# Kernel tuning notes

Measured on AMD Instinct MI355X. Metric: run time of the kernel, lower is better.

Reference implementation:

```python
import jax, jax.numpy as jnp
import numpy as np

EPS = 1e-6
HID = 2048; N_HEADS = 16; Q_LORA = 768; KV_LORA = 512
ROPE_D = 64; NOPE_D = 128; V_D = 128
IDX_H = 32; IDX_D = 128; IDX_TOPK = 512
N_EXP = 8; TOPK = 4; N_GROUP = 4; TOPK_GROUP = 2
MOE_I = 512; SHARED_I = 512; ROUTED_SCALE = 2.5
T = 1024
NEG = -1e30


def _rms(x, w, eps=EPS):
    x = x.astype(jnp.float32)
    return x * jax.lax.rsqrt(jnp.mean(x * x, axis=-1, keepdims=True) + eps) * w


def _ln(x, w, b, eps=EPS):
    x = x.astype(jnp.float32)
    m = jnp.mean(x, axis=-1, keepdims=True)
    v = jnp.mean((x - m) ** 2, axis=-1, keepdims=True)
    return (x - m) * jax.lax.rsqrt(v + eps) * w + b


def _rope_cs(positions, dim):
    inv = 1.0 / (10000.0 ** (jnp.arange(0, dim, 2, dtype=jnp.float32) / dim))
    f = positions.astype(jnp.float32)[:, None] * inv[None, :]  # [T, dim/2]
    return jnp.cos(f), jnp.sin(f)


def _rope(x, cos, sin):
    # neox-style rotate-half over last dim
    d = x.shape[-1] // 2
    x1, x2 = x[..., :d], x[..., d:]
    while cos.ndim < x.ndim:
        cos, sin = cos[:, None], sin[:, None]
    return jnp.concatenate([x1 * cos - x2 * sin, x2 * cos + x1 * sin], axis=-1)


def setup_inputs() -> dict:
    key = jax.random.key(0)
    ks = iter(jax.random.split(key, 32))
    w = lambda *s: jax.random.normal(next(ks), s, jnp.float32) * 0.02
    inp = {
        'positions': jnp.arange(T, dtype=jnp.int32),
        'hidden_states': jax.random.normal(next(ks), (T, HID), jnp.float32),
        'residual': jax.random.normal(next(ks), (T, HID), jnp.float32),
        'w_input_ln': jnp.ones((HID,), jnp.float32),
        'w_post_ln': jnp.ones((HID,), jnp.float32),
        'w_step1': w(Q_LORA + KV_LORA + ROPE_D + IDX_D + IDX_H, HID),
        'w_q_a_ln': jnp.ones((Q_LORA,), jnp.float32),
        'w_kv_a_ln': jnp.ones((KV_LORA,), jnp.float32),
        'idx_k_ln_w': jnp.ones((IDX_D,), jnp.float32),
        'idx_k_ln_b': jnp.zeros((IDX_D,), jnp.float32),
        'w_step3': w(IDX_H * IDX_D + N_HEADS * (NOPE_D + ROPE_D), Q_LORA),
        'W_UK_T': w(N_HEADS, NOPE_D, KV_LORA),
        'W_UV': w(N_HEADS, KV_LORA, V_D),
        'w_o': w(HID, N_HEADS * V_D),
        'gate_w': w(N_EXP, HID),
        'gate_bias': jnp.zeros((N_EXP,), jnp.float32),
        'shared_gate_up': w(2 * SHARED_I, HID),
        'shared_down': w(HID, SHARED_I),
        'exp_gate_up': w(N_EXP, 2 * MOE_I, HID),
        'exp_down': w(N_EXP, HID, MOE_I),
    }
    return inp


def reference(positions, hidden_states, residual, w_input_ln, w_post_ln, w_step1,
              w_q_a_ln, w_kv_a_ln, idx_k_ln_w, idx_k_ln_b, w_step3, W_UK_T, W_UV,
              w_o, gate_w, gate_bias, shared_gate_up, shared_down, exp_gate_up, exp_down):
    Tn = hidden_states.shape[0]
    rows = jnp.arange(Tn)
    # (allreduce is identity at tp=1) + residual add + RMSNorm
    res = hidden_states.astype(jnp.float32) + residual.astype(jnp.float32)
    h = _rms(res, w_input_ln)
    # ---- Step 1: fused qkv_a + indexer_wk + indexer_weights_proj GEMM ----
    s1 = h @ w_step1.T
    o0 = 0
    q_c = s1[:, o0:o0 + Q_LORA]; o0 += Q_LORA
    kv_c = s1[:, o0:o0 + KV_LORA]; o0 += KV_LORA
    k_pe = s1[:, o0:o0 + ROPE_D]; o0 += ROPE_D
    idx_k = s1[:, o0:o0 + IDX_D]; o0 += IDX_D
    idx_w_raw = s1[:, o0:o0 + IDX_H]
    cos, sin = _rope_cs(positions, ROPE_D)
    # fused_norm_rope: norms + rope on k_pe / indexer-k
    q_c = _rms(q_c, w_q_a_ln)
    kv_c = _rms(kv_c, w_kv_a_ln)
    k_pe = _rope(k_pe, cos, sin)
    idx_k = _ln(idx_k, idx_k_ln_w, idx_k_ln_b)
    idx_k = jnp.concatenate([_rope(idx_k[:, :ROPE_D], cos, sin), idx_k[:, ROPE_D:]], axis=-1)
    # ---- Step 3: fused indexer_wq_b + q_b_proj GEMM ----
    s3 = q_c @ w_step3.T
    idx_q = s3[:, :IDX_H * IDX_D].reshape(Tn, IDX_H, IDX_D)
    q = s3[:, IDX_H * IDX_D:].reshape(Tn, N_HEADS, NOPE_D + ROPE_D)
    q_nope, q_pe = q[..., :NOPE_D], q[..., NOPE_D:]
    # absorb W_UK: [T,H,nope] x [H,nope,kv_lora] -> [T,H,kv_lora]
    ql_nope = jnp.einsum('thn,hnk->thk', q_nope, W_UK_T)
    q_pe = _rope(q_pe, cos, sin)
    idx_q = jnp.concatenate([_rope(idx_q[..., :ROPE_D], cos, sin), idx_q[..., ROPE_D:]], axis=-1)
    idx_q = idx_q * (IDX_D ** -0.5)            # indexer softmax scale
    idx_w = idx_w_raw * (IDX_H ** -0.5)        # per-head weights scale
    # ---- sparse attention indexer: relu(q.k) head-weighted sum, causal top-k ----
    il = jnp.einsum('thd,sd->ths', idx_q, idx_k)          # [T,Hi,S]
    iscores = jnp.einsum('ths,th->ts', jax.nn.relu(il), idx_w)
    causal = positions[:, None] >= positions[None, :]
    iscores = jnp.where(causal, iscores, NEG)
    topk_idx = jax.lax.top_k(iscores, IDX_TOPK)[1]        # [T, IDX_TOPK]
    tmask = jnp.zeros((Tn, Tn), bool).at[rows[:, None], topk_idx].set(True)
    mask = causal & tmask
    # ---- MLA MQA attention in latent space ----
    mqa_q = jnp.concatenate([ql_nope, jnp.broadcast_to(q_pe, (Tn, N_HEADS, ROPE_D))], axis=-1)
    kv = jnp.concatenate([kv_c, k_pe], axis=-1)           # [S, kv_lora+rope]
    att = jnp.einsum('thd,sd->hts', mqa_q, kv) * ((NOPE_D + ROPE_D) ** -0.5)
    att = jnp.where(mask[None], att, NEG)
    p = jax.nn.softmax(att, axis=-1)
    o = jnp.einsum('hts,sk->thk', p, kv_c)                # [T,H,kv_lora]
    o = jnp.einsum('thk,hkv->thv', o, W_UV).reshape(Tn, N_HEADS * V_D)
    attn_out = o @ w_o.T
    # add + RMSNorm
    res2 = attn_out + res
    h2 = _rms(res2, w_post_ln)
    # ---- MoE: DeepSeekV3 sigmoid grouped routing + shared experts ----
    glog = h2 @ gate_w.T
    sg = jax.nn.sigmoid(glog)
    sc = sg + gate_bias
    gsz = N_EXP // N_GROUP
    grp = sc.reshape(Tn, N_GROUP, gsz)
    grp_score = jax.lax.top_k(grp, min(2, gsz))[0].sum(-1)
    gidx = jax.lax.top_k(grp_score, TOPK_GROUP)[1]
    gmask = jnp.zeros((Tn, N_GROUP), bool).at[rows[:, None], gidx].set(True)
    emask = jnp.repeat(gmask, gsz, axis=1)
    sc_m = jnp.where(emask, sc, NEG)
    _, tid = jax.lax.top_k(sc_m, TOPK)
    tw = jnp.take_along_axis(sg, tid, axis=1)
    tw = tw / (tw.sum(-1, keepdims=True) + 1e-20) * ROUTED_SCALE
    comb = jnp.zeros((Tn, N_EXP), jnp.float32).at[rows[:, None], tid].set(tw)
    # routed experts (dense masked combine as reference for grouped-GEMM dispatch)
    gu = jnp.einsum('th,eih->tei', h2, exp_gate_up)       # [T,E,2I]
    act = jax.nn.silu(gu[..., :MOE_I]) * gu[..., MOE_I:]
    routed_e = jnp.einsum('tei,ehi->teh', act, exp_down)  # [T,E,H]
    routed = jnp.einsum('te,teh->th', comb, routed_e)
    # shared experts
    gus = h2 @ shared_gate_up.T
    shared = (jax.nn.silu(gus[:, :SHARED_I]) * gus[:, SHARED_I:]) @ shared_down.T
    out = shared + routed
    return out, res2
```

## Files before the change

### kernel.cpp

```cpp
#include <hip/hip_runtime.h>
#include <math.h>

static constexpr int TT  = 1024;
static constexpr int HID = 2048;
static constexpr int NH  = 16;
static constexpr int QL  = 768;
static constexpr int KVL = 512;
static constexpr int RD  = 64;
static constexpr int IH  = 32;
static constexpr int ID  = 128;
static constexpr int S1W = QL + KVL + RD + ID + IH;
static constexpr int S3W = IH*ID + NH*(128+RD);

#define SCALE_ATT 0.07216878364870323f
#define SC_IDXQ   0.08838834764831845f
#define SC_IDXW   0.17677669529663687f
#define NEGR      -1e30f
#define NEGL      -3.0e38f

typedef __bf16 bf16x8 __attribute__((ext_vector_type(8)));
typedef float  f32x4  __attribute__((ext_vector_type(4)));

#define GLD_LDS16(g, l) __builtin_amdgcn_global_load_lds( \
    (const __attribute__((address_space(1))) void*)(g),   \
    (__attribute__((address_space(3))) void*)(l), 16, 0, 0)

__device__ __forceinline__ unsigned short f2b(float x) {
  union { float f; unsigned u; } v; v.f = x;
  unsigned r = v.u + 0x7FFFu + ((v.u >> 16) & 1u);
  return (unsigned short)(r >> 16);
}
__device__ __forceinline__ float b2f(unsigned short u) {
  union { unsigned u; float f; } v; v.u = ((unsigned)u) << 16;
  return v.f;
}

__device__ __forceinline__ float blk_sum256(float v, float* s) {
  #pragma unroll
  for (int o = 32; o > 0; o >>= 1) v += __shfl_down(v, o, 64);
  __syncthreads();
  if ((threadIdx.x & 63) == 0) s[threadIdx.x >> 6] = v;
  __syncthreads();
  return s[0] + s[1] + s[2] + s[3];
}

__global__ __launch_bounds__(256) void k_prelude(const float* __restrict__ hs,
                                                 const float* __restrict__ rsd,
                                                 const float* __restrict__ w,
                                                 float* __restrict__ res,
                                                 unsigned short* __restrict__ hb) {
  int t = blockIdx.x;
  __shared__ float scr[4];
  float vals[8]; float ss = 0.f;
  #pragma unroll
  for (int r = 0; r < 8; r++) {
    int d = threadIdx.x + 256*r;
    float v = hs[(size_t)t*HID + d] + rsd[(size_t)t*HID + d];
    vals[r] = v; res[(size_t)t*HID + d] = v; ss = fmaf(v, v, ss);
  }
  ss = blk_sum256(ss, scr);
  float inv = 1.f/sqrtf(ss/(float)HID + 1e-6f);
  #pragma unroll
  for (int r = 0; r < 8; r++) {
    int d = threadIdx.x + 256*r;
    hb[(size_t)t*HID + d] = f2b(vals[r]*inv*w[d]);
  }
}

__global__ __launch_bounds__(256) void k_res2(const float* __restrict__ attn1,
                                              const float* __restrict__ attn2,
                                              const float* __restrict__ res,
                                              const float* __restrict__ w,
                                              float* __restrict__ res2_out,
                                              float* __restrict__ h2,
                                              unsigned short* __restrict__ h2b) {
  int t = blockIdx.x;
  __shared__ float scr[4];
  float vals[8]; float ss = 0.f;
  #pragma unroll
  for (int r = 0; r < 8; r++) {
    int d = threadIdx.x + 256*r;
    float v = attn1[(size_t)t*HID + d] + attn2[(size_t)t*HID + d] + res[(size_t)t*HID + d];
    vals[r] = v; res2_out[(size_t)t*HID + d] = v; ss = fmaf(v, v, ss);
  }
  ss = blk_sum256(ss, scr);
  float inv = 1.f/sqrtf(ss/(float)HID + 1e-6f);
  #pragma unroll
  for (int r = 0; r < 8; r++) {
    int d = threadIdx.x + 256*r;
    float o = vals[r]*inv*w[d];
    h2[(size_t)t*HID + d] = o;
    h2b[(size_t)t*HID + d] = f2b(o);
  }
}

__global__ void k_ropecs(const int* __restrict__ pos, float* __restrict__ cosb, float* __restrict__ sinb) {
  int i = blockIdx.x*256 + threadIdx.x;
  if (i >= TT*32) return;
  int t = i >> 5, k = i & 31;
  double inv = pow(10000.0, -((double)(2*k))/64.0);
  double f = (double)pos[t] * inv;
  cosb[i] = (float)cos(f);
  sinb[i] = (float)sin(f);
}

__global__ void k_f2b(const float* __restrict__ s, unsigned short* __restrict__ d,
                      long long n, long long ntot) {
  long long stride = (long long)gridDim.x * 1024;
  for (long long i = ((long long)blockIdx.x*256 + threadIdx.x)*4; i < ntot; i += stride) {
    float x0, x1, x2, x3;
    if (i + 3 < n) { float4 v = *(const float4*)(s + i); x0=v.x; x1=v.y; x2=v.z; x3=v.w; }
    else {
      x0 = (i   < n) ? s[i]   : 0.f; x1 = (i+1 < n) ? s[i+1] : 0.f;
      x2 = (i+2 < n) ? s[i+2] : 0.f; x3 = (i+3 < n) ? s[i+3] : 0.f;
    }
    ushort4 o; o.x=f2b(x0); o.y=f2b(x1); o.z=f2b(x2); o.w=f2b(x3);
    *(ushort4*)(d + i) = o;
  }
}

__global__ void k_f2b4(const float* __restrict__ s0, unsigned short* __restrict__ d0, long long n0,
                       const float* __restrict__ s1, unsigned short* __restrict__ d1, long long n1,
                       const float* __restrict__ s2, unsigned short* __restrict__ d2, long long n2,
                       const float* __restrict__ s3, unsigned short* __restrict__ d3, long long n3) {
  long long ntot = n0 + n1 + n2 + n3;
  long long stride = (long long)gridDim.x * 1024;
  for (long long i = ((long long)blockIdx.x*256 + threadIdx.x)*4; i < ntot; i += stride) {
    const float* s; unsigned short* d; long long j = i;
    if (j < n0) { s = s0; d = d0; }
    else { j -= n0;
      if (j < n1) { s = s1; d = d1; }
      else { j -= n1;
        if (j < n2) { s = s2; d = d2; }
        else { j -= n2; s = s3; d = d3; } } }
    float4 v = *(const float4*)(s + j);
    ushort4 o; o.x=f2b(v.x); o.y=f2b(v.y); o.z=f2b(v.z); o.w=f2b(v.w);
    *(ushort4*)(d + j) = o;
  }
}

__global__ __launch_bounds__(256) void k_tconvb(const float* __restrict__ src,
                                                unsigned short* __restrict__ dst,
                                                int R, int C) {
  src += (size_t)blockIdx.z * R * C;
  dst += (size_t)blockIdx.z * R * C;
  __shared__ float tile[32][33];
  int c0 = blockIdx.x * 32, r0 = blockIdx.y * 32;
  int tx = threadIdx.x & 31, ty = threadIdx.x >> 5;
  #pragma unroll
  for (int i = 0; i < 4; i++) {
    int r = r0 + ty + i*8;
    tile[ty + i*8][tx] = src[(size_t)r*C + c0 + tx];
  }
  __syncthreads();
  #pragma unroll
  for (int i = 0; i < 4; i++) {
    int c = c0 + ty + i*8;
    dst[(size_t)c*R + r0 + tx] = f2b(tile[tx][ty + i*8]);
  }
}

template<int BM, int OUT, bool ILV, int MOE>
__global__ __launch_bounds__(256) void k_mgemm(
    const unsigned short* __restrict__ A, int lda, long long sA,
    const unsigned short* __restrict__ B, int ldb, long long sB,
    void* __restrict__ Cv, int ldc, long long sC,
    int N, int K, float alpha, int cskip, int ktri,
    int nseg, long long segA, long long segB,
    const float* __restrict__ comb,
    const int* __restrict__ cntp, const int* __restrict__ tokp) {
  constexpr int MR  = BM / 32;
  constexpr int ITA = BM / 32;
  const int row0 = blockIdx.y * BM;
  const int col0 = blockIdx.x * 128;
  if (cskip >= 0 && col0 > row0 + cskip) return;
  const int zb = blockIdx.z;
  int cnt = 0; long long off = 0;
  if (MOE) {
    cnt = cntp[zb];
    for (int e = 0; e < zb; e++) off += cntp[e];
    if (row0 >= cnt) return;
  }
  __shared__ __align__(16) unsigned short As[2][BM*64];
  __shared__ __align__(16) unsigned short Bs[2][128*64];
  const int tid  = threadIdx.x;
  const int wave = tid >> 6, lane = tid & 63;
  const int wm = wave >> 1, wn = wave & 1;
  A += (size_t)zb * (size_t)sA;
  B += (size_t)zb * (size_t)sB;
  if (MOE == 2) A += off * (long long)lda;

  int tki[ITA];
  if (MOE == 1) {
    #pragma unroll
    for (int it = 0; it < ITA; it++) {
      int r = (wave*64 + it*256 + lane) >> 3;
      tki[it] = tokp[zb*1024 + row0 + r];
    }
  }

  f32x4 acc[MR][4] = {};
  const int l15 = lane & 15, l4 = lane >> 4;
  const int sx = l15 & 7;
  int Kend = K;
  if (ktri) {
    int kub = (((row0 + BM - 1) >> 7) + 1) << 7;
    if (kub < Kend) Kend = kub;
  }
  const int nk = Kend >> 6;
  const int nt = nseg * nk;

  auto STAGE = [&](int b, const unsigned short* Ab, const unsigned short* Bb, int k0) {
    #pragma unroll
    for (int it = 0; it < ITA; it++) {
      int base = wave*64 + it*256;
      int sidx = base + lane;
      int r = sidx >> 3, s = sidx & 7;
      int s_src = s ^ (r & 7);
      const unsigned short* ga;
      if (MOE == 1) ga = Ab + (size_t)tki[it]*lda + k0 + s_src*8;
      else          ga = Ab + (size_t)(row0 + r)*lda + k0 + s_src*8;
      GLD_LDS16(ga, &As[b][base*8]);
    }
    #pragma unroll
    for (int it = 0; it < 4; it++) {
      int base = wave*64 + it*256;
      int sidx = base + lane;
      int r = sidx >> 3, s = sidx & 7;
      int s_src = s ^ (r & 7);
      int rt = col0 + r;
      int srow = ILV ? ((rt >> 1) + (rt & 1)*512) : rt;
      const unsigned short* gb = Bb + (size_t)srow*ldb + k0 + s_src*8;
      GLD_LDS16(gb, &Bs[b][base*8]);
    }
  };

  STAGE(0, A, B, 0);
  int ks = 64, sg = 0;
  if (ks == Kend) { ks = 0; sg = 1; }
  __syncthreads();
  int cur = 0;

  for (int u = 0; u < nt; u++) {
    if (u + 1 < nt) {
      STAGE(cur ^ 1, A + (size_t)sg*segA, B + (size_t)sg*segB, ks);
      ks += 64;
      if (ks == Kend) { ks = 0; sg++; }
    }
    #pragma unroll
    for (int kc = 0; kc < 2; kc++) {
      const int sl = ((kc*4 + l4) ^ sx) << 3;
      bf16x8 fa[MR], fb[4];
      #pragma unroll
      for (int mf = 0; mf < MR; mf++)
        fa[mf] = *(const bf16x8*)&As[cur][(wm*(BM/2) + mf*16 + l15)*64 + sl];
      #pragma unroll
      for (int nf = 0; nf < 4; nf++)
        fb[nf] = *(const bf16x8*)&Bs[cur][(wn*64 + nf*16 + l15)*64 + sl];
      #pragma unroll
      for (int mf = 0; mf < MR; mf++)
        #pragma unroll
        for (int nf = 0; nf < 4; nf++)
          acc[mf][nf] = __builtin_amdgcn_mfma_f32_16x16x32_bf16(fa[mf], fb[nf], acc[mf][nf], 0, 0, 0);
    }
    __syncthreads();
    cur ^= 1;
  }

  #pragma unroll
  for (int mf = 0; mf < MR; mf++) {
    #pragma unroll
    for (int nf = 0; nf < 4; nf++) {
      int n = col0 + wn*64 + nf*16 + l15;
      #pragma unroll
      for (int r = 0; r < 4; r++) {
        int m = row0 + wm*(BM/2) + mf*16 + l4*4 + r;
        float v = acc[mf][nf][r] * alpha;
        if (OUT == 2) {
          float p = __shfl_xor(v, 1, 64);
          if ((l15 & 1) == 0) {
            bool ok = true;
            long long mrow = m;
            float w;
            if (MOE == 1) {
              ok = (m < cnt); mrow = off + m;
              int tok = tokp[zb*1024 + m];
              w = (zb < 8) ? comb[tok*8 + zb] : 1.f;
            } else {
              w = (zb < 8) ? comb[m*8 + zb] : 1.f;
            }
            if (ok) {
              float rres = v/(1.f + expf(-v)) * p * w;
              ((unsigned short*)Cv)[(size_t)zb*sC + (size_t)mrow*ldc + (n >> 1)] = f2b(rres);
            }
          }
        } else if (n < N) {
          bool ok = true;
          long long mrow = m;
          if (MOE == 2) { ok = (m < cnt); mrow = off + m; }
          if (ok) {
            size_t idx = (size_t)mrow*ldc + n;
            if (OUT == 1) ((unsigned short*)Cv)[(size_t)zb*sC + idx] = f2b(v);
            else          ((float*)Cv)[(size_t)zb*sC + idx] = v;
          }
        }
      }
    }
  }
}

__global__ __launch_bounds__(256) void k_post1(const float* __restrict__ s1a,
    const float* __restrict__ s1b,
    const float* __restrict__ wq, const float* __restrict__ wkv,
    const float* __restrict__ lnw, const float* __restrict__ lnb,
    const float* __restrict__ cosb, const float* __restrict__ sinb,
    unsigned short* __restrict__ qcb, float* __restrict__ kvc, float* __restrict__ kpe,
    float* __restrict__ idxk, float* __restrict__ idxw) {
  int t = blockIdx.x, tid = threadIdx.x;
  __shared__ float rowb[S1W];
  __shared__ float scr[4];
  __shared__ float yb[128];
  for (int d = tid; d < S1W; d += 256)
    rowb[d] = s1a[(size_t)t*S1W + d] + s1b[(size_t)t*S1W + d];
  __syncthreads();
  float ss = 0.f;
  for (int d = tid; d < QL; d += 256) { float v = rowb[d]; ss = fmaf(v,v,ss); }
  ss = blk_sum256(ss, scr);
  float inv = 1.f/sqrtf(ss/(float)QL + 1e-6f);
  for (int d = tid; d < QL; d += 256) qcb[(size_t)t*QL + d] = f2b(rowb[d]*inv*wq[d]);
  ss = 0.f;
  for (int d = tid; d < KVL; d += 256) { float v = rowb[QL+d]; ss = fmaf(v,v,ss); }
  ss = blk_sum256(ss, scr);
  inv = 1.f/sqrtf(ss/(float)KVL + 1e-6f);
  for (int d = tid; d < KVL; d += 256) kvc[(size_t)t*KVL + d] = rowb[QL+d]*inv*wkv[d];
  float sm = (tid < 128) ? rowb[1344 + tid] : 0.f;
  float tot = blk_sum256(sm, scr);
  float mean = tot / 128.f;
  float vs = 0.f;
  if (tid < 128) { float v = rowb[1344+tid] - mean; vs = v*v; }
  vs = blk_sum256(vs, scr);
  float ivn = 1.f/sqrtf(vs/128.f + 1e-6f);
  if (tid < 128) yb[tid] = (rowb[1344+tid]-mean)*ivn*lnw[tid] + lnb[tid];
  __syncthreads();
  if (tid < 32) {
    float c = cosb[t*32 + tid], s = sinb[t*32 + tid];
    idxk[(size_t)t*ID + tid]      = yb[tid]*c - yb[32+tid]*s;
    idxk[(size_t)t*ID + 32 + tid] = yb[32+tid]*c + yb[tid]*s;
    float x1 = rowb[1280+tid], x2 = rowb[1312+tid];
    kpe[(size_t)t*RD + tid]      = x1*c - x2*s;
    kpe[(size_t)t*RD + 32 + tid] = x2*c + x1*s;
    idxw[(size_t)t*IH + tid] = rowb[1472+tid] * SC_IDXW;
  } else if (tid >= 64 && tid < 128) {
    idxk[(size_t)t*ID + tid] = yb[tid];
  }
}

__global__ __launch_bounds__(256) void k_post3b(const float* __restrict__ s3,
                                                const float* __restrict__ cosb,
                                                const float* __restrict__ sinb,
                                                unsigned short* __restrict__ s3b) {
  int t = blockIdx.x, tid = threadIdx.x;
  const float* row = s3 + (size_t)t*S3W;
  __shared__ float buf[S3W];
  __shared__ float cs[32], sn[32];
  if (tid < 32) { cs[tid] = cosb[t*32+tid]; sn[tid] = sinb[t*32+tid]; }
  for (int d = tid; d < S3W; d += 256) buf[d] = row[d];
  __syncthreads();
  for (int p = tid; p < 1024; p += 256) {
    int h = p >> 5, d = p & 31;
    float c = cs[d], s = sn[d];
    float x1 = buf[h*ID + d], x2 = buf[h*ID + 32 + d];
    buf[h*ID + d]      = (x1*c - x2*s) * SC_IDXQ;
    buf[h*ID + 32 + d] = (x2*c + x1*s) * SC_IDXQ;
  }
  for (int p = tid; p < 2048; p += 256) {
    int h = p >> 6, d = 64 + (p & 63);
    buf[h*ID + d] *= SC_IDXQ;
  }
  for (int p = tid; p < 512; p += 256) {
    int h = p >> 5, d = p & 31;
    float c = cs[d], s = sn[d];
    int base = IH*ID + h*192 + 128;
    float x1 = buf[base + d], x2 = buf[base + 32 + d];
    buf[base + d]      = x1*c - x2*s;
    buf[base + 32 + d] = x2*c + x1*s;
  }
  __syncthreads();
  unsigned short* orow = s3b + (size_t)t*S3W;
  for (int g = tid*4; g < S3W; g += 1024) {
    ushort4 o;
    o.x = f2b(buf[g]); o.y = f2b(buf[g+1]); o.z = f2b(buf[g+2]); o.w = f2b(buf[g+3]);
    *(ushort4*)(orow + g) = o;
  }
}

__global__ void k_qpe(const unsigned short* __restrict__ s3b, unsigned short* __restrict__ qm) {
  int i = blockIdx.x*256 + threadIdx.x;
  int t = i >> 10, r = i & 1023;
  int h = r >> 6, j = r & 63;
  float v = b2f(s3b[(size_t)t*S3W + IH*ID + h*192 + 128 + j]) * SCALE_ATT;
  qm[(size_t)t*9216 + h*576 + 512 + j] = f2b(v);
}

__global__ void k_kvb(const float* __restrict__ kvc, const float* __restrict__ kpe,
                      unsigned short* __restrict__ kvb) {
  int i = blockIdx.x*256 + threadIdx.x;
  int s = i / 576, d = i - s*576;
  float v = (d < 512) ? kvc[(size_t)s*KVL + d] : kpe[(size_t)s*RD + (d - 512)];
  kvb[i] = f2b(v);
}

__global__ __launch_bounds__(256) void k_ired(const float* __restrict__ il,
                                              const float* __restrict__ idxw,
                                              float* __restrict__ isc,
                                              int first, int last, int h0) {
  int tr = blockIdx.x;
  int t = 512 + tr;
  int s0 = threadIdx.x * 4;
  float4 acc;
  if (first) acc = make_float4(0.f, 0.f, 0.f, 0.f);
  else       acc = *(float4*)(isc + (size_t)tr*TT + s0);
  #pragma unroll
  for (int hh = 0; hh < 8; hh++) {
    float w = idxw[t*IH + h0 + hh];
    float4 v = *(const float4*)(il + (size_t)hh*524288 + (size_t)tr*1024 + s0);
    acc.x += fmaxf(v.x, 0.f) * w;
    acc.y += fmaxf(v.y, 0.f) * w;
    acc.z += fmaxf(v.z, 0.f) * w;
    acc.w += fmaxf(v.w, 0.f) * w;
  }
  if (last) {
    if (s0     > t) acc.x = NEGR;
    if (s0 + 1 > t) acc.y = NEGR;
    if (s0 + 2 > t) acc.z = NEGR;
    if (s0 + 3 > t) acc.w = NEGR;
  }
  *(float4*)(isc + (size_t)tr*TT + s0) = acc;
}

__global__ __launch_bounds__(512) void k_topk(const float* __restrict__ isc,
                                              unsigned char* __restrict__ mask) {
  int t = 512 + blockIdx.x;
  const float* row = isc + (size_t)blockIdx.x * TT;
  __shared__ unsigned long long keys[1024];
  int tid = threadIdx.x;
  for (int i = tid; i < 1024; i += 512) {
    float v = row[i];
    unsigned int b = __float_as_uint(v);
    unsigned int u = (b & 0x80000000u) ? ~b : (b | 0x80000000u);
    keys[i] = ((unsigned long long)u << 32) | (unsigned int)(1023 - i);
  }
  __syncthreads();
  for (int k = 2; k <= 1024; k <<= 1) {
    for (int j = k >> 1; j > 0; j >>= 1) {
      int i = ((tid & ~(j - 1)) << 1) | (tid & (j - 1));
      int l = i | j;
      unsigned long long a = keys[i], b = keys[l];
      bool up = ((i & k) == 0);
      if ((a < b) == up) { keys[i] = b; keys[l] = a; }
      __syncthreads();
    }
  }
  unsigned char* mrow = mask + (size_t)t * TT;
  for (int p = tid; p < 1024; p += 512) {
    int s = 1023 - (int)(keys[p] & 0xFFFFFFFFu);
    mrow[s] = (p < 512) ? (unsigned char)1 : (unsigned char)0;
  }
}

__global__ __launch_bounds__(256) void k_psoft(unsigned short* __restrict__ pb,
                                               const unsigned char* __restrict__ mask) {
  int b = blockIdx.x;
  int t = b & 1023, h = b >> 10;
  unsigned short* row = pb + ((size_t)h << 20) + ((size_t)t << 10);
  int tid = threadIdx.x;
  __shared__ float scr[4];
  int s0 = tid * 4;
  int rub = ((t >> 7) + 1) << 7;
  bool act = (s0 < rub);
  float v0 = 0.f, v1 = 0.f, v2 = 0.f, v3 = 0.f;
  bool m0 = false, m1 = false, m2 = false, m3 = false;
  if (act) {
    ushort4 raw = *(const ushort4*)(row + s0);
    v0 = b2f(raw.x); v1 = b2f(raw.y); v2 = b2f(raw.z); v3 = b2f(raw.w);
    if (t < 512) {
      m0 = (s0 <= t); m1 = (s0+1 <= t); m2 = (s0+2 <= t); m3 = (s0+3 <= t);
    } else {
      uchar4 mk = *(const uchar4*)(mask + (size_t)t*TT + s0);
      m0 = (s0 <= t) && mk.x; m1 = (s0+1 <= t) && mk.y;
      m2 = (s0+2 <= t) && mk.z; m3 = (s0+3 <= t) && mk.w;
    }
  }
  float mx = NEGL;
  if (m0) mx = v0;
  if (m1) mx = fmaxf(mx, v1);
  if (m2) mx = fmaxf(mx, v2);
  if (m3) mx = fmaxf(mx, v3);
  #pragma unroll
  for (int o = 32; o > 0; o >>= 1) mx = fmaxf(mx, __shfl_down(mx, o, 64));
  __syncthreads();
  if ((tid & 63) == 0) scr[tid >> 6] = mx;
  __syncthreads();
  mx = fmaxf(fmaxf(scr[0], scr[1]), fmaxf(scr[2], scr[3]));
  float p0 = m0 ? expf(v0 - mx) : 0.f;
  float p1 = m1 ? expf(v1 - mx) : 0.f;
  float p2 = m2 ? expf(v2 - mx) : 0.f;
  float p3 = m3 ? expf(v3 - mx) : 0.f;
  float sum = blk_sum256((p0+p1)+(p2+p3), scr);
  float inv = 1.f / sum;
  if (act) {
    ushort4 o;
    o.x = f2b(p0*inv); o.y = f2b(p1*inv); o.z = f2b(p2*inv); o.w = f2b(p3*inv);
    *(ushort4*)(row + s0) = o;
  }
}

__global__ __launch_bounds__(256) void k_gate(const float* __restrict__ h2,
                                              const float* __restrict__ gw,
                                              const float* __restrict__ gb,
                                              float* __restrict__ comb) {
  int t = blockIdx.x, tid = threadIdx.x;
  int e = tid >> 5, lane = tid & 31;
  __shared__ float gl[8];
  float p = 0.f;
  for (int d = lane; d < HID; d += 32) p = fmaf(h2[(size_t)t*HID+d], gw[(size_t)e*HID+d], p);
  #pragma unroll
  for (int o = 16; o > 0; o >>= 1) p += __shfl_down(p, o, 32);
  if (lane == 0) gl[e] = p;
  __syncthreads();
  if (tid == 0) {
    float sg[8], sc[8];
    #pragma unroll
    for (int i = 0; i < 8; i++) { sg[i] = 1.f/(1.f+expf(-gl[i])); sc[i] = sg[i] + gb[i]; }
    float gs[4];
    #pragma unroll
    for (int g = 0; g < 4; g++) gs[g] = sc[2*g] + sc[2*g+1];
    int g0 = 0;
    for (int g = 1; g < 4; g++) if (gs[g] > gs[g0]) g0 = g;
    int g1 = -1;
    for (int g = 0; g < 4; g++) { if (g == g0) continue; if (g1 < 0 || gs[g] > gs[g1]) g1 = g; }
    float wsum = 1e-20f;
    #pragma unroll
    for (int i = 0; i < 8; i++) { int g = i >> 1; if (g == g0 || g == g1) wsum += sg[i]; }
    #pragma unroll
    for (int i = 0; i < 8; i++) { int g = i >> 1; comb[t*8+i] = (g == g0 || g == g1) ? sg[i]/wsum*2.5f : 0.f; }
  }
}

__global__ __launch_bounds__(1024) void k_route(const float* __restrict__ comb,
                                                int* __restrict__ tokidx,
                                                int* __restrict__ rank,
                                                int* __restrict__ cntp) {
  int e = blockIdx.x;
  int t = threadIdx.x;
  if (e == 8) {
    tokidx[8*1024 + t] = t;
    if (t == 0) cntp[8] = 1024;
    return;
  }
  int lane = t & 63, w = t >> 6;
  bool sel = comb[t*8 + e] != 0.0f;
  unsigned long long bal = __ballot(sel);
  int pw = __popcll(bal & ((1ull << lane) - 1ull));
  int wt = __popcll(bal);
  __shared__ int wsum[16];
  if (lane == 0) wsum[w] = wt;
  __syncthreads();
  int woff = 0, total = 0;
  #pragma unroll
  for (int i = 0; i < 16; i++) { int v = wsum[i]; if (i < w) woff += v; total += v; }
  int pos = woff + pw;
  rank[t*8 + e] = sel ? pos : -1;
  if (sel) tokidx[e*1024 + pos] = t;
  __syncthreads();
  if (t >= total) tokidx[e*1024 + t] = 0;
  if (t == 0) cntp[e] = total;
}

__global__ __launch_bounds__(256) void k_rsum(const float* __restrict__ dpc,
                                              const int* __restrict__ rank,
                                              const int* __restrict__ cntp,
                                              float* __restrict__ out) {
  int t = blockIdx.x;
  int d = threadIdx.x * 8;
  int offs[8]; int acc_off = 0;
  #pragma unroll
  for (int e = 0; e < 8; e++) { offs[e] = acc_off; acc_off += cntp[e]; }
  const float* ps = dpc + (size_t)(acc_off + t)*2048 + d;
  float4 a0 = *(const float4*)ps;
  float4 a1 = *(const float4*)(ps + 4);
  #pragma unroll
  for (int e = 0; e < 8; e++) {
    int r = rank[t*8 + e];
    if (r >= 0) {
      const float* p = dpc + (size_t)(offs[e] + r)*2048 + d;
      float4 b0 = *(const float4*)p;
      float4 b1 = *(const float4*)(p + 4);
      a0.x += b0.x; a0.y += b0.y; a0.z += b0.z; a0.w += b0.w;
      a1.x += b1.x; a1.y += b1.y; a1.z += b1.z; a1.w += b1.w;
    }
  }
  float* po = out + (size_t)t*2048 + d;
  *(float4*)po = a0;
  *(float4*)(po + 4) = a1;
}

extern "C" void kernel_launch(void* const* d_in, const int* in_sizes, int n_in,
                              void* d_out, int out_size, void* d_ws, size_t ws_size,
                              hipStream_t stream) {
  const int*   positions = (const int*)d_in[0];
  const float* hs     = (const float*)d_in[1];
  const float* rsd    = (const float*)d_in[2];
  const float* w_in   = (const float*)d_in[3];
  const float* w_post = (const float*)d_in[4];
  const float* w_s1   = (const float*)d_in[5];
  const float* w_qln  = (const float*)d_in[6];
  const float* w_kvln = (const float*)d_in[7];
  const float* iklnw  = (const float*)d_in[8];
  const float* iklnb  = (const float*)d_in[9];
  const float* w_s3   = (const float*)d_in[10];
  const float* wukt   = (const float*)d_in[11];
  const float* wuv    = (const float*)d_in[12];
  const float* w_o    = (const float*)d_in[13];
  const float* gate_w = (const float*)d_in[14];
  const float* gate_b = (const float*)d_in[15];
  const float* sh_gu  = (const float*)d_in[16];
  const float* sh_dn  = (const float*)d_in[17];
  const float* ex_gu  = (const float*)d_in[18];
  const float* ex_dn  = (const float*)d_in[19];

  float* ws = (float*)d_ws;
  typedef unsigned short ush;
  float* RES   = ws + 0;
  float* COSB  = ws + 2097152;
  float* SINB  = ws + 2129920;
  float* KVC   = ws + 2162688;
  float* KPE   = ws + 2686976;
  float* IDXK  = ws + 2752512;
  float* IDXW  = ws + 2883584;
  float* COMB  = ws + 2916352;
  ush*   HB    = (ush*)(ws + 2924544);
  ush*   WS1B  = (ush*)(ws + 3973120);
  float* S1P0  = ws + 5545984;
  ush*   QCB   = (ush*)(ws + 7086080);
  ush*   WS3B  = (ush*)(ws + 7479296);
  ush*   WOB   = (ush*)(ws + 7479296);
  float* S3    = ws + 10231808;
  float* S1P1  = ws + 10231808;
  ush*   S3B   = (ush*)(ws + 17571840);
  ush*   WUKTB = (ush*)(ws + 21241856);
  ush*   QMQAB = (ush*)(ws + 21766144);
  float* ISC   = ws + 26484736;
  unsigned char* MASK = (unsigned char*)(ws + 27009024);
  ush*   WUVB  = (ush*)(ws + 27271168);
  ush*   KVB   = (ush*)(ws + 27795456);
  ush*   VTB   = (ush*)(ws + 28090368);
  ush*   O2B   = (ush*)(ws + 28352512);
  float* ILB   = ws + 27795456;
  ush*   IDXKB = (ush*)(ws + 31989760);
  ush*   PB    = (ush*)(ws + 10231808);
  ush*   OHB   = (ush*)(ws + 18620416);
  float* ATTNP = ws + 10231808;
  float* H2     = ws + 2924544;
  ush*   H2B    = (ush*)(ws + 5021696);
  ush*   EXGUB  = (ush*)(ws + 6070272);
  ush*   SHGUB  = (ush*)(ws + 14458880);
  ush*   EXDNB  = (ush*)(ws + 15507456);
  ush*   SHDNB  = (ush*)(ws + 19701760);
  ush*   ACTC   = (ush*)(ws + 20226048);
  float* DPC    = ws + 21536768;
  int*   TOKIDX = (int*)(ws + 32022528);
  int*   RANK   = (int*)(ws + 32031744);
  int*   CNT    = (int*)(ws + 32039936);

  float* OUT0 = (float*)d_out;
  float* OUT_RES2 = OUT0 + (size_t)TT*HID;

  k_prelude<<<TT, 256, 0, stream>>>(hs, rsd, w_in, RES, HB);
  k_ropecs<<<(TT*32)/256, 256, 0, stream>>>(positions, COSB, SINB);
  k_f2b<<<1024, 256, 0, stream>>>(w_s1, WS1B, 3080192LL, 3145728LL);
  k_f2b<<<1024, 256, 0, stream>>>(w_s3, WS3B, 5505024LL, 5505024LL);
  k_tconvb<<<dim3(16,4,16), 256, 0, stream>>>(wukt, WUKTB, 128, 512);
  k_tconvb<<<dim3(4,16,16), 256, 0, stream>>>(wuv, WUVB, 512, 128);
  k_mgemm<64,0,false,0><<<dim3(12,16,2), 256, 0, stream>>>(
      HB, 2048, 1024, WS1B, 2048, 1024, S1P0, S1W, 4685824,
      1504, 1024, 1.f, -1, 0, 1, 0, 0, nullptr, nullptr, nullptr);
  k_post1<<<TT, 256, 0, stream>>>(S1P0, S1P1, w_qln, w_kvln, iklnw, iklnb, COSB, SINB, QCB, KVC, KPE, IDXK, IDXW);
  k_f2b<<<128, 256, 0, stream>>>(IDXK, IDXKB, 131072LL, 131072LL);
  k_mgemm<64,0,false,0><<<dim3(56,16,1), 256, 0, stream>>>(
      QCB, 768, 0, WS3B, 768, 0, S3, S3W, 0,
      S3W, 768, 1.f, -1, 0, 1, 0, 0, nullptr, nullptr, nullptr);
  k_post3b<<<TT, 256, 0, stream>>>(S3, COSB, SINB, (ush*)S3B);
  k_f2b<<<1024, 256, 0, stream>>>(w_o, WOB, 4194304LL, 4194304LL);
  k_mgemm<64,1,false,0><<<dim3(4,16,16), 256, 0, stream>>>(
      S3B + 4096, S3W, 192, WUKTB, 128, 65536, QMQAB, 9216, 576,
      512, 128, SCALE_ATT, -1, 0, 1, 0, 0, nullptr, nullptr, nullptr);
  k_qpe<<<4096, 256, 0, stream>>>(S3B, QMQAB);
  for (int c = 0; c < 4; c++) {
    k_mgemm<64,0,false,0><<<dim3(8,8,8), 256, 0, stream>>>(
        S3B + (size_t)512*S3W + c*1024, S3W, 128, IDXKB, 128, 0,
        ILB, 1024, 524288, 1024, 128, 1.f, 639, 0, 1, 0, 0, nullptr, nullptr, nullptr);
    k_ired<<<512, 256, 0, stream>>>(ILB, IDXW, ISC, c == 0, c == 3, c*8);
  }
  k_topk<<<512, 512, 0, stream>>>(ISC, MASK);
  k_kvb<<<2304, 256, 0, stream>>>(KVC, KPE, KVB);
  k_tconvb<<<dim3(16,32,1), 256, 0, stream>>>(KVC, VTB, 1024, 512);
  k_mgemm<64,1,false,0><<<dim3(8,16,16), 256, 0, stream>>>(
      QMQAB, 9216, 576, KVB, 576, 0, PB, 1024, 1048576,
      1024, 576, 1.f, 127, 0, 1, 0, 0, nullptr, nullptr, nullptr);
  k_psoft<<<16384, 256, 0, stream>>>(PB, MASK);
  k_mgemm<64,1,false,0><<<dim3(4,16,16), 256, 0, stream>>>(
      PB, 1024, 1048576, VTB, 1024, 0, OHB, 512, 524288,
      512, 1024, 1.f, -1, 1, 1, 0, 0, nullptr, nullptr, nullptr);
  k_mgemm<64,1,false,0><<<dim3(1,16,16), 256, 0, stream>>>(
      OHB, 512, 524288, WUVB, 512, 65536, O2B, 2048, 128,
      128, 512, 1.f, -1, 0, 1, 0, 0, nullptr, nullptr, nullptr);
  k_mgemm<64,0,false,0><<<dim3(16,16,2), 256, 0, stream>>>(
      O2B, 2048, 1024, WOB, 2048, 1024, ATTNP, 2048, 2097152,
      2048, 1024, 1.f, -1, 0, 1, 0, 0, nullptr, nullptr, nullptr);
  k_res2<<<TT, 256, 0, stream>>>(ATTNP, ATTNP + 2097152, RES, w_post, OUT_RES2, H2, H2B);
  k_gate<<<TT, 256, 0, stream>>>(H2, gate_w, gate_b, COMB);
  k_route<<<9, 1024, 0, stream>>>(COMB, TOKIDX, RANK, CNT);
  k_f2b4<<<2048, 256, 0, stream>>>(ex_gu, EXGUB, 16777216LL,
                                   sh_gu, SHGUB, 2097152LL,
                                   ex_dn, EXDNB, 8388608LL,
                                   sh_dn, SHDNB, 1048576LL);
  k_mgemm<64,2,true,1><<<dim3(8,16,9), 256, 0, stream>>>(
      H2B, 2048, 0, EXGUB, 2048, 2097152, ACTC, 512, 0,
      1024, 2048, 1.f, -1, 0, 1, 0, 0, COMB, CNT, TOKIDX);
  k_mgemm<64,0,false,2><<<dim3(16,16,9), 256, 0, stream>>>(
      ACTC, 512, 0, EXDNB, 512, 1048576, DPC, 2048, 0,
      2048, 512, 1.f, -1, 0, 1, 0, 0, nullptr, CNT, nullptr);
  k_rsum<<<TT, 256, 0, stream>>>(DPC, RANK, CNT, OUT0);
}
```

Measured before the change: 446.5 us.

## Fuse indexer score reduction into GEMM, enlarge row tiles, store expert down-proj in bf16

The four-chunk indexer GEMM plus k_ired reduction is replaced by a single GEMM variant (OUT==3). It loops over all 32 heads as K segments, applies ReLU and the per-head weight in registers, writes the causal-masked score directly, and fills fully skipped tiles with the mask value. Most other GEMMs move from 64-row to 128-row tiles to improve operand reuse. The MoE down-projection now writes bf16 instead of fp32, and k_rsum reads bf16. The changes cut the fp32 intermediate traffic and launch count, at the cost of fewer blocks for the fused indexer GEMM (64) and lower precision in the routed partial sums.

```diff
diff --git a/kernel.cpp b/kernel.cpp
--- a/kernel.cpp
+++ b/kernel.cpp
@@ -173,7 +173,18 @@
   constexpr int ITA = BM / 32;
   const int row0 = blockIdx.y * BM;
   const int col0 = blockIdx.x * 128;
-  if (cskip >= 0 && col0 > row0 + cskip) return;
+  const int tid  = threadIdx.x;
+  if (cskip >= 0 && col0 > row0 + cskip) {
+    if (OUT == 3) {
+      float* C = (float*)Cv;
+      for (int i = tid; i < BM*32; i += 256) {
+        int rr = i >> 5, cc = (i & 31) * 4;
+        float4 ng = make_float4(NEGR, NEGR, NEGR, NEGR);
+        *(float4*)&C[(size_t)(row0 + rr)*ldc + col0 + cc] = ng;
+      }
+    }
+    return;
+  }
   const int zb = blockIdx.z;
   int cnt = 0; long long off = 0;
   if (MOE) {
@@ -183,13 +194,18 @@
   }
   __shared__ __align__(16) unsigned short As[2][BM*64];
   __shared__ __align__(16) unsigned short Bs[2][128*64];
-  const int tid  = threadIdx.x;
+  __shared__ float wlds[(OUT == 3) ? BM*32 : 1];
   const int wave = tid >> 6, lane = tid & 63;
   const int wm = wave >> 1, wn = wave & 1;
   A += (size_t)zb * (size_t)sA;
   B += (size_t)zb * (size_t)sB;
   if (MOE == 2) A += off * (long long)lda;
 
+  if constexpr (OUT == 3) {
+    for (int i = tid; i < BM*32; i += 256)
+      wlds[i] = comb[(size_t)(row0 + (i >> 5))*32 + (i & 31)];
+  }
+
   int tki[ITA];
   if (MOE == 1) {
     #pragma unroll
@@ -200,6 +216,7 @@
   }
 
   f32x4 acc[MR][4] = {};
+  f32x4 acc2[(OUT == 3) ? MR : 1][4] = {};
   const int l15 = lane & 15, l4 = lane >> 4;
   const int sx = l15 & 7;
   int Kend = K;
@@ -263,6 +280,24 @@
         for (int nf = 0; nf < 4; nf++)
           acc[mf][nf] = __builtin_amdgcn_mfma_f32_16x16x32_bf16(fa[mf], fb[nf], acc[mf][nf], 0, 0, 0);
     }
+    if constexpr (OUT == 3) {
+      if ((u + 1) % nk == 0) {
+        int h = u / nk;
+        #pragma unroll
+        for (int mf = 0; mf < MR; mf++) {
+          #pragma unroll
+          for (int r = 0; r < 4; r++) {
+            int rl = wm*(BM/2) + mf*16 + l4*4 + r;
+            float w = wlds[rl*32 + h];
+            #pragma unroll
+            for (int nf = 0; nf < 4; nf++) {
+              acc2[mf][nf][r] += fmaxf(acc[mf][nf][r], 0.f) * w;
+              acc[mf][nf][r] = 0.f;
+            }
+          }
+        }
+      }
+    }
     __syncthreads();
     cur ^= 1;
   }
@@ -275,6 +310,12 @@
       #pragma unroll
       for (int r = 0; r < 4; r++) {
         int m = row0 + wm*(BM/2) + mf*16 + l4*4 + r;
+        if (OUT == 3) {
+          float v = acc2[mf][nf][r];
+          if (n > 512 + m) v = NEGR;
+          ((float*)Cv)[(size_t)m*ldc + n] = v;
+          continue;
+        }
         float v = acc[mf][nf][r] * alpha;
         if (OUT == 2) {
           float p = __shfl_xor(v, 1, 64);
@@ -410,34 +451,6 @@
   kvb[i] = f2b(v);
 }
 
-__global__ __launch_bounds__(256) void k_ired(const float* __restrict__ il,
-                                              const float* __restrict__ idxw,
-                                              float* __restrict__ isc,
-                                              int first, int last, int h0) {
-  int tr = blockIdx.x;
-  int t = 512 + tr;
-  int s0 = threadIdx.x * 4;
-  float4 acc;
-  if (first) acc = make_float4(0.f, 0.f, 0.f, 0.f);
-  else       acc = *(float4*)(isc + (size_t)tr*TT + s0);
-  #pragma unroll
-  for (int hh = 0; hh < 8; hh++) {
-    float w = idxw[t*IH + h0 + hh];
-    float4 v = *(const float4*)(il + (size_t)hh*524288 + (size_t)tr*1024 + s0);
-    acc.x += fmaxf(v.x, 0.f) * w;
-    acc.y += fmaxf(v.y, 0.f) * w;
-    acc.z += fmaxf(v.z, 0.f) * w;
-    acc.w += fmaxf(v.w, 0.f) * w;
-  }
-  if (last) {
-    if (s0     > t) acc.x = NEGR;
-    if (s0 + 1 > t) acc.y = NEGR;
-    if (s0 + 2 > t) acc.z = NEGR;
-    if (s0 + 3 > t) acc.w = NEGR;
-  }
-  *(float4*)(isc + (size_t)tr*TT + s0) = acc;
-}
-
 __global__ __launch_bounds__(512) void k_topk(const float* __restrict__ isc,
                                               unsigned char* __restrict__ mask) {
   int t = 512 + blockIdx.x;
@@ -577,7 +590,7 @@
   if (t == 0) cntp[e] = total;
 }
 
-__global__ __launch_bounds__(256) void k_rsum(const float* __restrict__ dpc,
+__global__ __launch_bounds__(256) void k_rsum(const unsigned short* __restrict__ dpc,
                                               const int* __restrict__ rank,
                                               const int* __restrict__ cntp,
                                               float* __restrict__ out) {
@@ -586,23 +599,26 @@
   int offs[8]; int acc_off = 0;
   #pragma unroll
   for (int e = 0; e < 8; e++) { offs[e] = acc_off; acc_off += cntp[e]; }
-  const float* ps = dpc + (size_t)(acc_off + t)*2048 + d;
-  float4 a0 = *(const float4*)ps;
-  float4 a1 = *(const float4*)(ps + 4);
+  const unsigned short* ps = dpc + (size_t)(acc_off + t)*2048 + d;
+  ushort4 u0 = *(const ushort4*)ps;
+  ushort4 u1 = *(const ushort4*)(ps + 4);
+  float a[8];
+  a[0]=b2f(u0.x); a[1]=b2f(u0.y); a[2]=b2f(u0.z); a[3]=b2f(u0.w);
+  a[4]=b2f(u1.x); a[5]=b2f(u1.y); a[6]=b2f(u1.z); a[7]=b2f(u1.w);
   #pragma unroll
   for (int e = 0; e < 8; e++) {
     int r = rank[t*8 + e];
     if (r >= 0) {
-      const float* p = dpc + (size_t)(offs[e] + r)*2048 + d;
-      float4 b0 = *(const float4*)p;
-      float4 b1 = *(const float4*)(p + 4);
-      a0.x += b0.x; a0.y += b0.y; a0.z += b0.z; a0.w += b0.w;
-      a1.x += b1.x; a1.y += b1.y; a1.z += b1.z; a1.w += b1.w;
+      const unsigned short* p = dpc + (size_t)(offs[e] + r)*2048 + d;
+      ushort4 b0 = *(const ushort4*)p;
+      ushort4 b1 = *(const ushort4*)(p + 4);
+      a[0]+=b2f(b0.x); a[1]+=b2f(b0.y); a[2]+=b2f(b0.z); a[3]+=b2f(b0.w);
+      a[4]+=b2f(b1.x); a[5]+=b2f(b1.y); a[6]+=b2f(b1.z); a[7]+=b2f(b1.w);
     }
   }
   float* po = out + (size_t)t*2048 + d;
-  *(float4*)po = a0;
-  *(float4*)(po + 4) = a1;
+  *(float4*)po       = make_float4(a[0], a[1], a[2], a[3]);
+  *(float4*)(po + 4) = make_float4(a[4], a[5], a[6], a[7]);
 }
 
 extern "C" void kernel_launch(void* const* d_in, const int* in_sizes, int n_in,
@@ -656,7 +672,6 @@
   ush*   KVB   = (ush*)(ws + 27795456);
   ush*   VTB   = (ush*)(ws + 28090368);
   ush*   O2B   = (ush*)(ws + 28352512);
-  float* ILB   = ws + 27795456;
   ush*   IDXKB = (ush*)(ws + 31989760);
   ush*   PB    = (ush*)(ws + 10231808);
   ush*   OHB   = (ush*)(ws + 18620416);
@@ -668,7 +683,7 @@
   ush*   EXDNB  = (ush*)(ws + 15507456);
   ush*   SHDNB  = (ush*)(ws + 19701760);
   ush*   ACTC   = (ush*)(ws + 20226048);
-  float* DPC    = ws + 21536768;
+  ush*   DPC    = (ush*)(ws + 21536768);
   int*   TOKIDX = (int*)(ws + 32022528);
   int*   RANK   = (int*)(ws + 32031744);
   int*   CNT    = (int*)(ws + 32039936);
@@ -682,40 +697,38 @@
   k_f2b<<<1024, 256, 0, stream>>>(w_s3, WS3B, 5505024LL, 5505024LL);
   k_tconvb<<<dim3(16,4,16), 256, 0, stream>>>(wukt, WUKTB, 128, 512);
   k_tconvb<<<dim3(4,16,16), 256, 0, stream>>>(wuv, WUVB, 512, 128);
-  k_mgemm<64,0,false,0><<<dim3(12,16,2), 256, 0, stream>>>(
+  k_mgemm<128,0,false,0><<<dim3(12,8,2), 256, 0, stream>>>(
       HB, 2048, 1024, WS1B, 2048, 1024, S1P0, S1W, 4685824,
       1504, 1024, 1.f, -1, 0, 1, 0, 0, nullptr, nullptr, nullptr);
   k_post1<<<TT, 256, 0, stream>>>(S1P0, S1P1, w_qln, w_kvln, iklnw, iklnb, COSB, SINB, QCB, KVC, KPE, IDXK, IDXW);
   k_f2b<<<128, 256, 0, stream>>>(IDXK, IDXKB, 131072LL, 131072LL);
-  k_mgemm<64,0,false,0><<<dim3(56,16,1), 256, 0, stream>>>(
+  k_mgemm<128,0,false,0><<<dim3(56,8,1), 256, 0, stream>>>(
       QCB, 768, 0, WS3B, 768, 0, S3, S3W, 0,
       S3W, 768, 1.f, -1, 0, 1, 0, 0, nullptr, nullptr, nullptr);
   k_post3b<<<TT, 256, 0, stream>>>(S3, COSB, SINB, (ush*)S3B);
   k_f2b<<<1024, 256, 0, stream>>>(w_o, WOB, 4194304LL, 4194304LL);
-  k_mgemm<64,1,false,0><<<dim3(4,16,16), 256, 0, stream>>>(
+  k_mgemm<128,1,false,0><<<dim3(4,8,16), 256, 0, stream>>>(
       S3B + 4096, S3W, 192, WUKTB, 128, 65536, QMQAB, 9216, 576,
       512, 128, SCALE_ATT, -1, 0, 1, 0, 0, nullptr, nullptr, nullptr);
   k_qpe<<<4096, 256, 0, stream>>>(S3B, QMQAB);
-  for (int c = 0; c < 4; c++) {
-    k_mgemm<64,0,false,0><<<dim3(8,8,8), 256, 0, stream>>>(
-        S3B + (size_t)512*S3W + c*1024, S3W, 128, IDXKB, 128, 0,
-        ILB, 1024, 524288, 1024, 128, 1.f, 639, 0, 1, 0, 0, nullptr, nullptr, nullptr);
-    k_ired<<<512, 256, 0, stream>>>(ILB, IDXW, ISC, c == 0, c == 3, c*8);
-  }
+  k_mgemm<64,3,false,0><<<dim3(8,8,1), 256, 0, stream>>>(
+      S3B + (size_t)512*S3W, S3W, 0, IDXKB, 128, 0,
+      ISC, 1024, 0, 1024, 128, 1.f, 575, 0, 32, 128, 0,
+      IDXW + (size_t)512*IH, nullptr, nullptr);
   k_topk<<<512, 512, 0, stream>>>(ISC, MASK);
   k_kvb<<<2304, 256, 0, stream>>>(KVC, KPE, KVB);
   k_tconvb<<<dim3(16,32,1), 256, 0, stream>>>(KVC, VTB, 1024, 512);
-  k_mgemm<64,1,false,0><<<dim3(8,16,16), 256, 0, stream>>>(
+  k_mgemm<128,1,false,0><<<dim3(8,8,16), 256, 0, stream>>>(
       QMQAB, 9216, 576, KVB, 576, 0, PB, 1024, 1048576,
       1024, 576, 1.f, 127, 0, 1, 0, 0, nullptr, nullptr, nullptr);
   k_psoft<<<16384, 256, 0, stream>>>(PB, MASK);
-  k_mgemm<64,1,false,0><<<dim3(4,16,16), 256, 0, stream>>>(
+  k_mgemm<128,1,false,0><<<dim3(4,8,16), 256, 0, stream>>>(
       PB, 1024, 1048576, VTB, 1024, 0, OHB, 512, 524288,
       512, 1024, 1.f, -1, 1, 1, 0, 0, nullptr, nullptr, nullptr);
-  k_mgemm<64,1,false,0><<<dim3(1,16,16), 256, 0, stream>>>(
+  k_mgemm<128,1,false,0><<<dim3(1,8,16), 256, 0, stream>>>(
       OHB, 512, 524288, WUVB, 512, 65536, O2B, 2048, 128,
       128, 512, 1.f, -1, 0, 1, 0, 0, nullptr, nullptr, nullptr);
-  k_mgemm<64,0,false,0><<<dim3(16,16,2), 256, 0, stream>>>(
+  k_mgemm<128,0,false,0><<<dim3(16,8,2), 256, 0, stream>>>(
       O2B, 2048, 1024, WOB, 2048, 1024, ATTNP, 2048, 2097152,
       2048, 1024, 1.f, -1, 0, 1, 0, 0, nullptr, nullptr, nullptr);
   k_res2<<<TT, 256, 0, stream>>>(ATTNP, ATTNP + 2097152, RES, w_post, OUT_RES2, H2, H2B);
@@ -725,10 +738,10 @@
                                    sh_gu, SHGUB, 2097152LL,
                                    ex_dn, EXDNB, 8388608LL,
                                    sh_dn, SHDNB, 1048576LL);
-  k_mgemm<64,2,true,1><<<dim3(8,16,9), 256, 0, stream>>>(
+  k_mgemm<128,2,true,1><<<dim3(8,8,9), 256, 0, stream>>>(
       H2B, 2048, 0, EXGUB, 2048, 2097152, ACTC, 512, 0,
       1024, 2048, 1.f, -1, 0, 1, 0, 0, COMB, CNT, TOKIDX);
-  k_mgemm<64,0,false,2><<<dim3(16,16,9), 256, 0, stream>>>(
+  k_mgemm<128,1,false,2><<<dim3(16,8,9), 256, 0, stream>>>(
       ACTC, 512, 0, EXDNB, 512, 1048576, DPC, 2048, 0,
       2048, 512, 1.f, -1, 0, 1, 0, 0, nullptr, CNT, nullptr);
   k_rsum<<<TT, 256, 0, stream>>>(DPC, RANK, CNT, OUT0);
```

Measured after the change: 426.9 us. -4.4%, faster.
